# Kernel tuning notes

Measured on AMD Instinct MI355X. Metric: run time of the kernel, lower is better.

Reference implementation:

```python
import jax, jax.numpy as jnp
import numpy as np

INPUT, HIDDEN, OUTPUT = 512, 1024, 512
BATCH, SEQ = 128, 256


def setup_inputs() -> dict:
    key = jax.random.key(0)
    ks = jax.random.split(key, 14)
    s_in = 1.0 / np.sqrt(INPUT)
    s_h = 1.0 / np.sqrt(HIDDEN)
    d = {
        "x_seq": jax.random.normal(ks[0], (BATCH, SEQ, INPUT), jnp.float32),
        "Wxf_w": jax.random.uniform(ks[1], (HIDDEN, INPUT), jnp.float32, -s_in, s_in),
        "Wxf_b": jax.random.uniform(ks[2], (HIDDEN,), jnp.float32, -s_in, s_in),
        "Whf_w": jax.random.uniform(ks[3], (HIDDEN, HIDDEN), jnp.float32, -s_h, s_h),
        "Wxi_w": jax.random.uniform(ks[4], (HIDDEN, INPUT), jnp.float32, -s_in, s_in),
        "Wxi_b": jax.random.uniform(ks[5], (HIDDEN,), jnp.float32, -s_in, s_in),
        "Whi_w": jax.random.uniform(ks[6], (HIDDEN, HIDDEN), jnp.float32, -s_h, s_h),
        "Wxg_w": jax.random.uniform(ks[7], (HIDDEN, INPUT), jnp.float32, -s_in, s_in),
        "Wxg_b": jax.random.uniform(ks[8], (HIDDEN,), jnp.float32, -s_in, s_in),
        "Whg_w": jax.random.uniform(ks[9], (HIDDEN, HIDDEN), jnp.float32, -s_h, s_h),
        "Wxo_w": jax.random.uniform(ks[10], (HIDDEN, INPUT), jnp.float32, -s_in, s_in),
        "Wxo_b": jax.random.uniform(ks[11], (HIDDEN,), jnp.float32, -s_in, s_in),
        "Who_w": jax.random.uniform(ks[12], (HIDDEN, HIDDEN), jnp.float32, -s_h, s_h),
        "Why_w": jax.random.uniform(ks[13], (OUTPUT, HIDDEN), jnp.float32, -s_h, s_h),
        "Why_b": jnp.zeros((OUTPUT,), jnp.float32),
    }
    return d


def _lstm(x_seq, Wxf_w, Wxf_b, Whf_w, Wxi_w, Wxi_b, Whi_w,
          Wxg_w, Wxg_b, Whg_w, Wxo_w, Wxo_b, Who_w, Why_w, Why_b):
    batch, seq_len, _ = x_seq.shape
    hidden = Whf_w.shape[0]
    # Precompute input projections for all timesteps (one big GEMM per gate).
    xf = jnp.einsum('bsi,hi->bsh', x_seq, Wxf_w) + Wxf_b  # (B,S,H)
    xi = jnp.einsum('bsi,hi->bsh', x_seq, Wxi_w) + Wxi_b
    xg = jnp.einsum('bsi,hi->bsh', x_seq, Wxg_w) + Wxg_b
    xo = jnp.einsum('bsi,hi->bsh', x_seq, Wxo_w) + Wxo_b
    # time-major for scan: (S, B, H)
    xs = jnp.stack([xf, xi, xg, xo], axis=0).transpose(2, 0, 1, 3)  # (S,4,B,H)

    h0 = jnp.zeros((batch, hidden), x_seq.dtype)
    c0 = jnp.zeros((batch, hidden), x_seq.dtype)

    def step(carry, x_t):
        h, c = carry
        xf_t, xi_t, xg_t, xo_t = x_t[0], x_t[1], x_t[2], x_t[3]
        f_t = jax.nn.sigmoid(xf_t + h @ Whf_w.T)
        i_t = jax.nn.sigmoid(xi_t + h @ Whi_w.T)
        g_t = jnp.tanh(xg_t + h @ Whg_w.T)
        c = f_t * c + i_t * g_t
        o_t = jax.nn.sigmoid(xo_t + h @ Who_w.T)
        h = o_t * jnp.tanh(c)
        return (h, c), None

    (h, c), _ = jax.lax.scan(step, (h0, c0), xs)
    out = h @ Why_w.T + Why_b
    return out, h, c


def reference(x_seq, Wxf_w, Wxf_b, Whf_w, Wxi_w, Wxi_b, Whi_w,
              Wxg_w, Wxg_b, Whg_w, Wxo_w, Wxo_b, Who_w, Why_w, Why_b):
    return _lstm(x_seq, Wxf_w, Wxf_b, Whf_w, Wxi_w, Wxi_b, Whi_w,
                 Wxg_w, Wxg_b, Whg_w, Wxo_w, Wxo_b, Who_w, Why_w, Why_b)
```

## Files before the change

kernel.cpp:

```cpp
#include <hip/hip_runtime.h>


#define B_ 128
#define S_ 256
#define I_ 512
#define H_ 1024
#define O_ 512

typedef unsigned short u16;
typedef unsigned int u32;
typedef unsigned long long u64;

typedef short v8s __attribute__((ext_vector_type(8)));
typedef float v16f __attribute__((ext_vector_type(16)));
typedef float v4f __attribute__((ext_vector_type(4)));

__device__ __forceinline__ u16 f2bf(float f) {
  u32 u = __float_as_uint(f);
  u32 r = (u + 0x7fffu + ((u >> 16) & 1u)) >> 16;
  return (u16)r;
}
__device__ __forceinline__ u32 pack2(float a, float b) {
  return (u32)f2bf(a) | ((u32)f2bf(b) << 16);
}
__device__ __forceinline__ uint4 cvt8(const float* __restrict__ s) {
  float4 f0 = ((const float4*)s)[0];
  float4 f1 = ((const float4*)s)[1];
  uint4 o;
  o.x = pack2(f0.x, f0.y); o.y = pack2(f0.z, f0.w);
  o.z = pack2(f1.x, f1.y); o.w = pack2(f1.z, f1.w);
  return o;
}

__device__ __forceinline__ uint4 uc_ld16(const u16* p) {
  u64 lo = __hip_atomic_load((const u64*)p, __ATOMIC_RELAXED, __HIP_MEMORY_SCOPE_AGENT);
  u64 hi = __hip_atomic_load((const u64*)p + 1, __ATOMIC_RELAXED, __HIP_MEMORY_SCOPE_AGENT);
  uint4 v; v.x = (u32)lo; v.y = (u32)(lo >> 32); v.z = (u32)hi; v.w = (u32)(hi >> 32);
  return v;
}
__device__ __forceinline__ void uc_st16(u16* p, uint4 v) {
  u64 lo = (u64)v.x | ((u64)v.y << 32);
  u64 hi = (u64)v.z | ((u64)v.w << 32);
  __hip_atomic_store((u64*)p, lo, __ATOMIC_RELAXED, __HIP_MEMORY_SCOPE_AGENT);
  __hip_atomic_store((u64*)p + 1, hi, __ATOMIC_RELAXED, __HIP_MEMORY_SCOPE_AGENT);
}

__global__ void lstm_prep(
    const float* __restrict__ x,
    const float* __restrict__ Whf, const float* __restrict__ Whi,
    const float* __restrict__ Whg, const float* __restrict__ Who,
    const float* __restrict__ Wxf, const float* __restrict__ Wxi,
    const float* __restrict__ Wxg, const float* __restrict__ Wxo,
    const float* __restrict__ bfp, const float* __restrict__ bip,
    const float* __restrict__ bgp, const float* __restrict__ bop,
    const float* __restrict__ Why,
    u16* __restrict__ xt, u16* __restrict__ Wc, float* __restrict__ bc,
    u16* __restrict__ WhyT, u16* __restrict__ hbuf, u32* __restrict__ barrier)
{
  const int gid = blockIdx.x * blockDim.x + threadIdx.x;
  const int gsz = gridDim.x * blockDim.x;

  if (gid < 1024) barrier[gid] = 0u;

  for (int v = gid; v < (S_ * B_ * I_ / 8); v += gsz) {
    int flat = v * 8;
    int b = flat / (S_ * I_);
    int rem = flat - b * (S_ * I_);
    int t = rem / I_;
    int i = rem - t * I_;
    size_t dst = ((size_t)(t * 4 + (b >> 5)) * 64 + (i >> 3)) * 32 + (b & 31);
    ((uint4*)xt)[dst] = cvt8(x + flat);
  }

  for (int o = gid; o < 192 * 4096; o += gsz) {
    int w8 = o >> 12;
    int colG = o & 4095;
    int unit = ((colG >> 6) << 4) + (((colG >> 5) & 1) << 3) + ((colG >> 2) & 7);
    int g = colG & 3;
    const float* Whp = (g == 0) ? Whf : (g == 1) ? Whi : (g == 2) ? Whg : Who;
    const float* Wxp = (g == 0) ? Wxf : (g == 1) ? Wxi : (g == 2) ? Wxg : Wxo;
    const float* s = (w8 < 64) ? (Wxp + (size_t)unit * 512 + w8 * 8)
                               : (Whp + (size_t)unit * 1024 + (w8 - 64) * 8);
    ((uint4*)Wc)[o] = cvt8(s);
  }

  for (int n = gid; n < 4096; n += gsz) {
    int unit = ((n >> 6) << 4) + (((n >> 5) & 1) << 3) + ((n >> 2) & 7);
    int g = n & 3;
    const float* bp = (g == 0) ? bfp : (g == 1) ? bip : (g == 2) ? bgp : bop;
    bc[n] = bp[unit];
  }

  for (int v = gid; v < (O_ * H_ / 8); v += gsz) {
    int flat = v * 8;
    *(uint4*)(WhyT + flat) = cvt8(Why + flat);
  }

  for (int v = gid; v < 2 * 16384; v += gsz) {
    uint4 z; z.x = 0; z.y = 0; z.z = 0; z.w = 0;
    ((uint4*)hbuf)[v] = z;
  }
}

__global__ __launch_bounds__(256, 1) void lstm_seq(
    const u16* __restrict__ xt, const u16* __restrict__ Wc,
    const float* __restrict__ bc, u16* __restrict__ hbuf,
    const u16* __restrict__ WhyT, const float* __restrict__ WhyB,
    float* __restrict__ out, u32* __restrict__ barrier, int rotFlag)
{
  __shared__ float scr[4096];
  __shared__ u16 hws[512];

  const int tid  = threadIdx.x;
  const int lane = tid & 63;
  const int w    = tid >> 6;
  const int ct   = w & 1;
  const int kh   = w >> 1;
  const int rq   = blockIdx.x >> 6;
  const int cg   = blockIdx.x & 63;
  const bool rot = (rotFlag != 0);

  const int colN  = lane & 31;
  const int kgsel = lane >> 5;
  const int colG  = cg * 64 + ct * 32 + colN;
  const int gate  = colN & 3;
  const int unitL = ct * 8 + (colN >> 2);
  const float bias = bc[colG];

  const uint4* xA4  = (const uint4*)xt;
  const uint4* WcF4 = (const uint4*)Wc;
  uint4*       HA4  = (uint4*)hbuf;

  const int xaOff = rq * 2048 + kh * 1024 + lane;
  const int xbOff = kh * 131072 + kgsel * 4096 + colG;
  const int haOff = rq * 4096 + kh * 2048 + lane;
  const int hbOff = 262144 + kh * 262144 + kgsel * 4096 + colG;

  float c[8];
#pragma unroll
  for (int i = 0; i < 8; ++i) c[i] = 0.f;

  __builtin_amdgcn_fence(__ATOMIC_ACQUIRE, "agent");
  __syncthreads();

  v8s Bx[16], Bh[32];
  {
    const uint4* bx = WcF4 + xbOff;
#pragma unroll
    for (int kb = 0; kb < 16; ++kb)
      Bx[kb] = __builtin_bit_cast(v8s, bx[(size_t)kb * 8192]);
    const uint4* bh = WcF4 + hbOff;
#pragma unroll
    for (int kb = 0; kb < 32; ++kb)
      Bh[kb] = __builtin_bit_cast(v8s, bh[(size_t)kb * 8192]);
  }

  v16f acc0, acc1;

#pragma unroll 1
  for (int t = 0; t < S_; ++t) {
    const size_t tb = rot ? (size_t)t * 16384 : (size_t)(t & 1) * 16384;
    const size_t tn = rot ? (size_t)(t + 1) * 16384 : (size_t)((t & 1) ^ 1) * 16384;

#pragma unroll
    for (int i = 0; i < 16; ++i) { acc0[i] = 0.f; acc1[i] = 0.f; }

    {
      const uint4* ax = xA4 + (size_t)t * 8192 + xaOff;
      v8s xr[16];
#pragma unroll
      for (int kb = 0; kb < 16; ++kb)
        xr[kb] = __builtin_bit_cast(v8s, ax[kb * 64]);
#pragma unroll
      for (int kb = 0; kb < 16; ++kb) {
        if (kb & 1) acc1 = __builtin_amdgcn_mfma_f32_32x32x16_bf16(xr[kb], Bx[kb], acc1, 0, 0, 0);
        else        acc0 = __builtin_amdgcn_mfma_f32_32x32x16_bf16(xr[kb], Bx[kb], acc0, 0, 0, 0);
      }
    }

    if (t > 0) {
      const u64* fb = (const u64*)(barrier + rq * 256 + kh * 128);
      u32 spins = 0;
      for (;;) {
        u64 v = __hip_atomic_load(fb + lane, __ATOMIC_RELAXED,
                                  __HIP_MEMORY_SCOPE_AGENT);
        if ((u32)v >= (u32)t && (u32)(v >> 32) >= (u32)t) break;
        __builtin_amdgcn_s_sleep(1);
        if (++spins > (1u << 22)) break;
      }
    }

    {
      const uint4* ah = HA4 + tb + haOff;
      v8s hr[32];
      if (rot) {
#pragma unroll
        for (int kb = 0; kb < 32; ++kb)
          hr[kb] = __builtin_bit_cast(v8s, ah[kb * 64]);
      } else {
#pragma unroll
        for (int kb = 0; kb < 32; ++kb)
          hr[kb] = __builtin_bit_cast(v8s, uc_ld16((const u16*)(ah + kb * 64)));
      }
#pragma unroll
      for (int kb = 0; kb < 32; ++kb) {
        if (kb & 1) acc1 = __builtin_amdgcn_mfma_f32_32x32x16_bf16(hr[kb], Bh[kb], acc1, 0, 0, 0);
        else        acc0 = __builtin_amdgcn_mfma_f32_32x32x16_bf16(hr[kb], Bh[kb], acc0, 0, 0, 0);
      }
    }

    float aT[16];
#pragma unroll
    for (int i = 0; i < 16; ++i) aT[i] = acc0[i] + acc1[i];
    float* scrT = scr + ((t & 1) << 11);
    {
      int h2 = 1 - kh;
#pragma unroll
      for (int i = 0; i < 8; ++i)
        scrT[ct * 1024 + h2 * 512 + i * 64 + lane] = aT[h2 * 8 + i];
    }
    __syncthreads();

    const bool lastT = (t == S_ - 1);
#pragma unroll
    for (int i = 0; i < 8; ++i) {
      int r = kh * 8 + i;
      float pre = aT[r] + scrT[ct * 1024 + kh * 512 + i * 64 + lane] + bias;
      float e = __expf((gate == 2) ? (2.f * pre) : (-pre));
      float act = (gate == 2) ? (1.f - 2.f / (e + 1.f)) : (1.f / (1.f + e));
      int qb = lane & ~3;
      float F = __shfl(act, qb + 0, 64);
      float I = __shfl(act, qb + 1, 64);
      float G = __shfl(act, qb + 2, 64);
      float O = __shfl(act, qb + 3, 64);
      float cn = fmaf(F, c[i], I * G);
      c[i] = cn;
      float e2 = __expf(2.f * cn);
      float hv = O * (1.f - 2.f / (e2 + 1.f));
      if (gate == 0) {
        int rowL = (r & 3) + ((r >> 2) << 3) + (kgsel << 2);
        hws[(w << 7) + ((rowL & 15) << 3) + (colN >> 2)] = f2bf(hv);
        if (lastT) {
          int grow = rq * 32 + rowL;
          int gunit = cg * 16 + unitL;
          out[65536 + grow * H_ + gunit] = hv;
          out[196608 + grow * H_ + gunit] = cn;
        }
      }
      if (lane < 2) {
        int R = (r & 3) + ((r >> 2) << 3) + (lane << 2);
        uint4 vv = *(const uint4*)(hws + (w << 7) + ((R & 15) << 3));
        uc_st16((u16*)(HA4 + tn + rq * 4096 + (size_t)(2 * cg + ct) * 32 + R), vv);
      }
    }

    asm volatile("s_waitcnt vmcnt(0)" ::: "memory");
    if (lane == 0)
      __hip_atomic_store(&barrier[rq * 256 + cg * 4 + w], (u32)(t + 1),
                         __ATOMIC_RELAXED, __HIP_MEMORY_SCOPE_AGENT);
  }

  {
    const u64* fb = (const u64*)barrier;
#pragma unroll 1
    for (int k = tid; k < 512; k += 256) {
      u32 spins = 0;
      for (;;) {
        u64 v = __hip_atomic_load(fb + k, __ATOMIC_RELAXED,
                                  __HIP_MEMORY_SCOPE_AGENT);
        if ((u32)v >= (u32)S_ && (u32)(v >> 32) >= (u32)S_) break;
        __builtin_amdgcn_s_sleep(2);
        if (++spins > (1u << 22)) break;
      }
    }
  }
  __syncthreads();

  if (blockIdx.x < 32) {
    const int wg = blockIdx.x;
    const uint4* HF = HA4 + (rot ? (size_t)S_ * 16384 : 0);
    const int l15 = lane & 15;
    const int l4 = lane >> 4;
    const int colO = (wg << 4) + l15;
    v4f o0, o1;
#pragma unroll
    for (int i = 0; i < 4; ++i) { o0[i] = 0.f; o1[i] = 0.f; }
#pragma unroll 4
    for (int kc = 0; kc < 32; ++kc) {
      v8s bfrag = *(const v8s*)(WhyT + (size_t)colO * H_ + kc * 32 + (l4 << 3));
      size_t i0 = (size_t)w * 4096 + kc * 128 + l4 * 32 + l15;
      v8s a0, a1;
      if (rot) {
        a0 = __builtin_bit_cast(v8s, HF[i0]);
        a1 = __builtin_bit_cast(v8s, HF[i0 + 16]);
      } else {
        a0 = __builtin_bit_cast(v8s, uc_ld16((const u16*)(HF + i0)));
        a1 = __builtin_bit_cast(v8s, uc_ld16((const u16*)(HF + i0 + 16)));
      }
      o0 = __builtin_amdgcn_mfma_f32_16x16x32_bf16(a0, bfrag, o0, 0, 0, 0);
      o1 = __builtin_amdgcn_mfma_f32_16x16x32_bf16(a1, bfrag, o1, 0, 0, 0);
    }
    float bO = WhyB[colO];
#pragma unroll
    for (int r2 = 0; r2 < 4; ++r2) {
      int row = (w << 5) + (l4 << 2) + r2;
      out[row * O_ + colO] = o0[r2] + bO;
      out[(row + 16) * O_ + colO] = o1[r2] + bO;
    }
  }
}

extern "C" void kernel_launch(void* const* d_in, const int* in_sizes, int n_in,
                              void* d_out, int out_size, void* d_ws, size_t ws_size,
                              hipStream_t stream) {
  const float* x    = (const float*)d_in[0];
  const float* Wxf  = (const float*)d_in[1];
  const float* bf_  = (const float*)d_in[2];
  const float* Whf  = (const float*)d_in[3];
  const float* Wxi  = (const float*)d_in[4];
  const float* bi_  = (const float*)d_in[5];
  const float* Whi  = (const float*)d_in[6];
  const float* Wxg  = (const float*)d_in[7];
  const float* bg_  = (const float*)d_in[8];
  const float* Whg  = (const float*)d_in[9];
  const float* Wxo  = (const float*)d_in[10];
  const float* bo_  = (const float*)d_in[11];
  const float* Who  = (const float*)d_in[12];
  const float* Why  = (const float*)d_in[13];
  const float* Whyb = (const float*)d_in[14];

  char* ws = (char*)d_ws;
  u16*   xtp  = (u16*)(ws);
  u16*   Wcp  = (u16*)(ws + 33554432);
  float* bcp  = (float*)(ws + 46137344);
  u16*   WhyT = (u16*)(ws + 46153728);
  u32*   barp = (u32*)(ws + 47202304);
  u16*   hbuf = (u16*)(ws + 47206400);
  float* outp = (float*)d_out;

  const size_t need_rot = 47206400ull + 257ull * 262144ull;
  int rot = (ws_size >= need_rot) ? 1 : 0;

  lstm_prep<<<dim3(1024), dim3(256), 0, stream>>>(
      x, Whf, Whi, Whg, Who, Wxf, Wxi, Wxg, Wxo,
      bf_, bi_, bg_, bo_, Why, xtp, Wcp, bcp, WhyT, hbuf, barp);

  lstm_seq<<<dim3(256), dim3(256), 0, stream>>>(
      xtp, Wcp, bcp, hbuf, WhyT, Whyb, outp, barp, rot);
}
```

Baseline: 2.477 ms.

## Aggregate per-wave barrier flags into one per-block flag via LDS counter

Each block now publishes one barrier flag per step instead of four. Its waves first bump a shared-memory counter after storing their h slices, and thread 0 spins on that counter before writing the global flag. Consumers then poll 16 u64 slots (32 flags) per wave instead of 64, and the final wait reads one flag per thread. The h write-back is also restructured so each wave writes 16 rows of its slice at once after the loop rather than 2 per iteration. The aim is less global flag traffic and polling cost on the critical recurrent path, at the cost of an intra-block serialization step before each publish.

```diff
diff --git a/kernel.cpp b/kernel.cpp
--- a/kernel.cpp
+++ b/kernel.cpp
@@ -110,6 +110,7 @@
 {
   __shared__ float scr[4096];
   __shared__ u16 hws[512];
+  __shared__ u32 pubcnt;
 
   const int tid  = threadIdx.x;
   const int lane = tid & 63;
@@ -140,6 +141,8 @@
 #pragma unroll
   for (int i = 0; i < 8; ++i) c[i] = 0.f;
 
+  if (tid == 0) pubcnt = 0u;
+
   __builtin_amdgcn_fence(__ATOMIC_ACQUIRE, "agent");
   __syncthreads();
 
@@ -179,12 +182,16 @@
     }
 
     if (t > 0) {
-      const u64* fb = (const u64*)(barrier + rq * 256 + kh * 128);
+      const u64* fb = (const u64*)(barrier + rq * 64 + kh * 32);
       u32 spins = 0;
       for (;;) {
-        u64 v = __hip_atomic_load(fb + lane, __ATOMIC_RELAXED,
-                                  __HIP_MEMORY_SCOPE_AGENT);
-        if ((u32)v >= (u32)t && (u32)(v >> 32) >= (u32)t) break;
+        int ok = 1;
+        if (lane < 16) {
+          u64 v = __hip_atomic_load(fb + lane, __ATOMIC_RELAXED,
+                                    __HIP_MEMORY_SCOPE_AGENT);
+          ok = ((u32)v >= (u32)t) && ((u32)(v >> 32) >= (u32)t);
+        }
+        if (__all(ok)) break;
         __builtin_amdgcn_s_sleep(1);
         if (++spins > (1u << 22)) break;
       }
@@ -247,31 +254,34 @@
           out[196608 + grow * H_ + gunit] = cn;
         }
       }
-      if (lane < 2) {
-        int R = (r & 3) + ((r >> 2) << 3) + (lane << 2);
-        uint4 vv = *(const uint4*)(hws + (w << 7) + ((R & 15) << 3));
-        uc_st16((u16*)(HA4 + tn + rq * 4096 + (size_t)(2 * cg + ct) * 32 + R), vv);
-      }
-    }
-
-    asm volatile("s_waitcnt vmcnt(0)" ::: "memory");
-    if (lane == 0)
-      __hip_atomic_store(&barrier[rq * 256 + cg * 4 + w], (u32)(t + 1),
-                         __ATOMIC_RELAXED, __HIP_MEMORY_SCOPE_AGENT);
+    }
+
+    {
+      if (lane < 16) {
+        uint4 vv = *(const uint4*)(hws + (w << 7) + (lane << 3));
+        uc_st16((u16*)(HA4 + tn + rq * 4096 + (size_t)(2 * cg + ct) * 32 +
+                       kh * 16 + lane), vv);
+      }
+      asm volatile("s_waitcnt vmcnt(0)" ::: "memory");
+      if (lane == 0) atomicAdd(&pubcnt, 1u);
+      if (tid == 0) {
+        u32 spins = 0;
+        while (__hip_atomic_load(&pubcnt, __ATOMIC_RELAXED,
+                                 __HIP_MEMORY_SCOPE_WORKGROUP) < 4u * (u32)(t + 1)) {
+          if (++spins > (1u << 24)) break;
+        }
+        __hip_atomic_store(&barrier[rq * 64 + cg], (u32)(t + 1), __ATOMIC_RELAXED,
+                           __HIP_MEMORY_SCOPE_AGENT);
+      }
+    }
   }
 
   {
-    const u64* fb = (const u64*)barrier;
-#pragma unroll 1
-    for (int k = tid; k < 512; k += 256) {
-      u32 spins = 0;
-      for (;;) {
-        u64 v = __hip_atomic_load(fb + k, __ATOMIC_RELAXED,
-                                  __HIP_MEMORY_SCOPE_AGENT);
-        if ((u32)v >= (u32)S_ && (u32)(v >> 32) >= (u32)S_) break;
-        __builtin_amdgcn_s_sleep(2);
-        if (++spins > (1u << 22)) break;
-      }
+    u32 spins = 0;
+    while (__hip_atomic_load(&barrier[tid], __ATOMIC_RELAXED,
+                             __HIP_MEMORY_SCOPE_AGENT) < (u32)S_) {
+      __builtin_amdgcn_s_sleep(2);
+      if (++spins > (1u << 22)) break;
     }
   }
   __syncthreads();
```

After: 2.362 ms. 4.6% less time.
